# Kernel optimization log

Hardware: AMD Instinct MI355X
Metric: run time of the kernel (lower is better)

## Reference

```python
import jax, jax.numpy as jnp
import numpy as np

D_MODEL = 512
NUM_HEADS = 8
HEAD_DIM = D_MODEL // NUM_HEADS
BATCH = 4
SEQ = 2048
ROPE_BASE = 10000.0


def rope_cos_sin(seq_len, head_dim):
    inv_freq = 1.0 / (ROPE_BASE ** (jnp.arange(0, head_dim, 2, dtype=jnp.float32) / head_dim))
    t = jnp.arange(seq_len, dtype=jnp.float32)
    freqs = jnp.outer(t, inv_freq)              # (S, head_dim/2)
    emb = jnp.concatenate([freqs, freqs], axis=-1)  # (S, head_dim)
    return jnp.cos(emb), jnp.sin(emb)


def apply_rope(x, cos, sin):
    # x: (..., S, head_dim); cos/sin: (S, head_dim)
    x1 = x[..., ::2]
    x2 = x[..., 1::2]
    ch = cos[..., ::2]
    sh = sin[..., ::2]
    r1 = x1 * ch - x2 * sh
    r2 = x1 * sh + x2 * ch
    return jnp.stack([r1, r2], axis=-1).reshape(x.shape)


def setup_inputs() -> dict:
    key = jax.random.key(0)
    ks = jax.random.split(key, 12)
    x = jax.random.normal(ks[0], (BATCH, SEQ, D_MODEL), dtype=jnp.float32)
    variate_ids = jnp.sort(jax.random.randint(ks[1], (BATCH, SEQ), 0, 8), axis=-1).astype(jnp.int64)
    mask = jnp.ones((BATCH, SEQ), dtype=jnp.float32)
    s = 1.0 / np.sqrt(D_MODEL)
    Wq = jax.random.normal(ks[2], (D_MODEL, D_MODEL), dtype=jnp.float32) * s
    bq = jnp.zeros((D_MODEL,), dtype=jnp.float32)
    Wk = jax.random.normal(ks[3], (D_MODEL, D_MODEL), dtype=jnp.float32) * s
    bk = jnp.zeros((D_MODEL,), dtype=jnp.float32)
    Wv = jax.random.normal(ks[4], (D_MODEL, D_MODEL), dtype=jnp.float32) * s
    bv = jnp.zeros((D_MODEL,), dtype=jnp.float32)
    Wo = jax.random.normal(ks[5], (D_MODEL, D_MODEL), dtype=jnp.float32) * s
    bo = jnp.zeros((D_MODEL,), dtype=jnp.float32)
    u_same = jax.random.normal(ks[6], (NUM_HEADS,), dtype=jnp.float32) * 0.1
    u_cross = jax.random.normal(ks[7], (NUM_HEADS,), dtype=jnp.float32) * 0.1
    return dict(x=x, variate_ids=variate_ids, mask=mask, Wq=Wq, bq=bq, Wk=Wk, bk=bk,
                Wv=Wv, bv=bv, Wo=Wo, bo=bo, u_same=u_same, u_cross=u_cross)


def reference(x, variate_ids, mask, Wq, bq, Wk, bk, Wv, bv, Wo, bo, u_same, u_cross):
    B, S, D = x.shape
    H, Hd = NUM_HEADS, HEAD_DIM
    scale = 1.0 / np.sqrt(Hd)

    def proj(W, b):
        return (x @ W.T + b).reshape(B, S, H, Hd).transpose(0, 2, 1, 3)  # (B,H,S,Hd)

    q = proj(Wq, bq)
    k = proj(Wk, bk)
    v = proj(Wv, bv)

    cos, sin = rope_cos_sin(S, Hd)
    q = apply_rope(q, cos, sin)
    k = apply_rope(k, cos, sin)

    scores = jnp.einsum('bhid,bhjd->bhij', q, k) * scale  # (B,H,S,S)
    same = (variate_ids[:, :, None] == variate_ids[:, None, :]).astype(jnp.float32)  # (B,S,S)
    bias = same[:, None] * u_same[None, :, None, None] + (1.0 - same)[:, None] * u_cross[None, :, None, None]
    scores = scores + bias
    scores = scores + (1.0 - mask[:, None, None, :]) * -1e9
    probs = jax.nn.softmax(scores, axis=-1)
    out = jnp.einsum('bhij,bhjd->bhid', probs, v)  # (B,H,S,Hd)
    out = out.transpose(0, 2, 1, 3).reshape(B, S, D)
    return out @ Wo.T + bo
```

## Files before the change

### kernel.cpp

```cpp
#include <hip/hip_runtime.h>
#include <hip/hip_bf16.h>

#define BATCH   4
#define SEQ     2048
#define DMODEL  512
#define NHEADS  8
#define HEADDIM 64
#define MTOT    (BATCH*SEQ)
#define NX      (MTOT*DMODEL)
#define NW      (DMODEL*DMODEL)
#define QTILE   64
#define KTILE   32
#define NKT_G   32

#define LOG2E   1.4426950408889634f
#define SCL2    0.18033688011112042f
#define SHIFT   14.426950408889634f

typedef unsigned short u16;
typedef __bf16 bf16x8 __attribute__((ext_vector_type(8)));
typedef float  f32x4  __attribute__((ext_vector_type(4)));
typedef unsigned short u16x4 __attribute__((ext_vector_type(4)));
typedef unsigned u32x2 __attribute__((ext_vector_type(2)));

#define MFMA(a,b,c) __builtin_amdgcn_mfma_f32_16x16x32_bf16(a,b,c,0,0,0)

__device__ __forceinline__ u16 f2bf(float f) {
    unsigned u = __float_as_uint(f);
    u += 0x7FFFu + ((u >> 16) & 1u);
    return (u16)(u >> 16);
}
__device__ __forceinline__ unsigned pk_bf16(float a, float b) {
    union { __hip_bfloat162 h; unsigned u; } cv;
    cv.h = __float22bfloat162_rn(make_float2(a, b));
    return cv.u;
}
__device__ __forceinline__ float qsum16(float v) {
    v += __shfl_xor(v, 1);
    v += __shfl_xor(v, 2);
    v += __shfl_xor(v, 4);
    v += __shfl_xor(v, 8);
    return v;
}
__device__ __forceinline__ void gll16(const void* g, void* l) {
    __builtin_amdgcn_global_load_lds((const __attribute__((address_space(1))) void*)g,
                                     (__attribute__((address_space(3))) void*)l, 16, 0, 0);
}
__device__ __forceinline__ void gll4(const void* g, void* l) {
    __builtin_amdgcn_global_load_lds((const __attribute__((address_space(1))) void*)g,
                                     (__attribute__((address_space(3))) void*)l, 4, 0, 0);
}

#define NCVT4 ((NX + 4*NW)/4)
__global__ __launch_bounds__(256) void cvt_rope_kernel(
    const float* __restrict__ x,
    const float* __restrict__ wq, const float* __restrict__ wk,
    const float* __restrict__ wv, const float* __restrict__ wo,
    u16* __restrict__ xbf,
    u16* __restrict__ wqbf, u16* __restrict__ wkbf,
    u16* __restrict__ wvbf, u16* __restrict__ wobf,
    float2* __restrict__ cst)
{
    int i4 = blockIdx.x * 256 + threadIdx.x;
    if (i4 < NCVT4) {
        int i = i4 * 4;
        const float* s; u16* d; int o;
        if (i < NX) { s = x; d = xbf; o = i; }
        else {
            int j = i - NX;
            int r = j >> 18;
            o = j & (NW - 1);
            s = (r == 0) ? wq : (r == 1) ? wk : (r == 2) ? wv : wo;
            d = (r == 0) ? wqbf : (r == 1) ? wkbf : (r == 2) ? wvbf : wobf;
        }
        float4 v = *(const float4*)(s + o);
        u16x4 u = { f2bf(v.x), f2bf(v.y), f2bf(v.z), f2bf(v.w) };
        *(u16x4*)(d + o) = u;
    } else {
        int r = i4 - NCVT4;
        if (r < SEQ * 32 / 4) {
            int idx = r * 4;
            int s  = idx >> 5;
            int p0 = idx & 31;
#pragma unroll
            for (int t = 0; t < 4; ++t) {
                int p = p0 + t;
                float inv = __expf(-0.5756462732485115f * (float)(p & 15));
                float ang = (float)s * inv;
                cst[idx + t] = make_float2(cosf(ang), sinf(ang));
            }
        }
    }
}

#define TP 136
__global__ __launch_bounds__(256) void qkv_kernel(
    const u16* __restrict__ x,
    const u16* __restrict__ Wq, const float* __restrict__ bq,
    const u16* __restrict__ Wk, const float* __restrict__ bk,
    const u16* __restrict__ Wv, const float* __restrict__ bv,
    const float* __restrict__ cstf,
    u16* __restrict__ qws, u16* __restrict__ kws, u16* __restrict__ vtws)
{
    __shared__ alignas(16) u16 smem[128 * TP];
    u16* As = smem;
    u16* Bs = smem + 8192;

    const int m0 = blockIdx.x * 128;
    const int n0 = blockIdx.y * 128;
    const int tid  = threadIdx.x;
    const int w    = tid >> 6;
    const int lane = tid & 63;
    const int quad = lane >> 4;
    const int l16  = lane & 15;
    const int wm = w & 1, wn = w >> 1;

    const int sec = n0 >> 9;
    const int oc0 = n0 & 511;
    const u16*   Wm = (sec == 0) ? Wq : (sec == 1 ? Wk : Wv);
    const float* bb = (sec == 0) ? bq : (sec == 1 ? bk : bv);

    const int xb = (sec < 2) ? wn : wm;
    const int wb = (sec < 2) ? wm : wn;

    f32x4 acc[4][4] = {};

    for (int kb = 0; kb < 8; ++kb) {
#pragma unroll
        for (int it = 0; it < 4; ++it) {
            const int s   = it * 256 + tid;
            const int row = s >> 3;
            const int cb  = s & 7;
            const int gcol = kb * 64 + (((cb ^ (row & 7))) << 3);
            gll16(x  + (m0  + row) * 512 + gcol, &As[s * 8]);
            gll16(Wm + (oc0 + row) * 512 + gcol, &Bs[s * 8]);
        }
        __syncthreads();

#pragma unroll
        for (int ks = 0; ks < 2; ++ks) {
            bf16x8 xf[4], wf[4];
#pragma unroll
            for (int t = 0; t < 4; ++t) {
                const int xrow = xb * 64 + t * 16 + l16;
                const int wrow = wb * 64 + t * 16 + l16;
                xf[t] = *(const bf16x8*)&As[xrow * 64 + (((ks * 4 + quad) ^ (xrow & 7)) << 3)];
                wf[t] = *(const bf16x8*)&Bs[wrow * 64 + (((ks * 4 + quad) ^ (wrow & 7)) << 3)];
            }
            if (sec < 2) {
#pragma unroll
                for (int tm = 0; tm < 4; ++tm)
#pragma unroll
                    for (int tn = 0; tn < 4; ++tn)
                        acc[tm][tn] = MFMA(wf[tm], xf[tn], acc[tm][tn]);
            } else {
#pragma unroll
                for (int tm = 0; tm < 4; ++tm)
#pragma unroll
                    for (int tn = 0; tn < 4; ++tn)
                        acc[tm][tn] = MFMA(xf[tm], wf[tn], acc[tm][tn]);
            }
        }
        __syncthreads();
    }

    if (sec < 2) {
#pragma unroll
        for (int tm = 0; tm < 4; ++tm) {
            const int dls = wm * 64 + tm * 16 + quad * 4;
            const float4 bv4 = *(const float4*)&bb[oc0 + dls];
            const int pbase = ((oc0 + dls) & 63) >> 1;
#pragma unroll
            for (int tn = 0; tn < 4; ++tn) {
                const int sl = wn * 64 + tn * 16 + l16;
                const int sg = (m0 + sl) & 2047;
                const float4 cs = *(const float4*)&cstf[sg * 64 + pbase * 2];
                const float v0 = acc[tm][tn][0] + bv4.x;
                const float v1 = acc[tm][tn][1] + bv4.y;
                const float v2 = acc[tm][tn][2] + bv4.z;
                const float v3 = acc[tm][tn][3] + bv4.w;
                const float r0 = v0 * cs.x - v1 * cs.y;
                const float r1 = v1 * cs.x + v0 * cs.y;
                const float r2 = v2 * cs.z - v3 * cs.w;
                const float r3 = v3 * cs.z + v2 * cs.w;
                u32x2 pv = { pk_bf16(r0, r1), pk_bf16(r2, r3) };
                *(u32x2*)&smem[sl * TP + dls] = pv;
            }
        }
        __syncthreads();
        u16* dst0 = (sec == 0) ? qws : kws;
#pragma unroll
        for (int i = 0; i < 8; ++i) {
            const int c   = i * 256 + tid;
            const int sl  = c >> 4;
            const int d8  = (c & 15) * 8;
            const int gcol = oc0 + d8;
            const int hh  = gcol >> 6;
            const int dh  = gcol & 63;
            const int sgl = m0 + sl;
            const int bi  = sgl >> 11;
            const int s   = sgl & 2047;
            u16* dst = dst0 + (size_t)(bi * NHEADS + hh) * (SEQ * HEADDIM)
                            + (size_t)s * HEADDIM + dh;
            *(bf16x8*)dst = *(const bf16x8*)&smem[sl * TP + d8];
        }
    } else {
#pragma unroll
        for (int tm = 0; tm < 4; ++tm) {
            const int row_l = wm * 64 + tm * 16 + quad * 4;
#pragma unroll
            for (int tn = 0; tn < 4; ++tn) {
                const int col_l = wn * 64 + tn * 16 + l16;
                const float bval = bb[oc0 + col_l];
                u32x2 pv = { pk_bf16(acc[tm][tn][0] + bval, acc[tm][tn][1] + bval),
                             pk_bf16(acc[tm][tn][2] + bval, acc[tm][tn][3] + bval) };
                *(u32x2*)&smem[col_l * TP + row_l] = pv;
            }
        }
        __syncthreads();
        const int bi  = m0 >> 11;
        const int sgb = m0 & 2047;
#pragma unroll
        for (int i = 0; i < 8; ++i) {
            const int c    = i * 256 + tid;
            const int col  = c >> 4;
            const int sc8  = (c & 15) * 8;
            const int gcol = oc0 + col;
            const int hh   = gcol >> 6;
            const int d    = gcol & 63;
            u16* dst = vtws + (size_t)(bi * NHEADS + hh) * (SEQ * HEADDIM)
                            + (size_t)d * SEQ + sgb + sc8;
            *(bf16x8*)dst = *(const bf16x8*)&smem[col * TP + sc8];
        }
    }
}

__global__ __launch_bounds__(512, 6) void attn_kernel(
    const u16* __restrict__ qws, const u16* __restrict__ kws,
    const u16* __restrict__ vtl,
    const int* __restrict__ vids, const float* __restrict__ mask,
    const float* __restrict__ u_same, const float* __restrict__ u_cross,
    u16* __restrict__ attn)
{
    __shared__ alignas(16) u16 smem[21504];
    __shared__ int   bidm[2][2][KTILE];
    __shared__ float bmkm[2][2][KTILE];
    __shared__ float comb_li[QTILE];

    const int bh = blockIdx.y;
    const int b  = bh >> 3;
    const int h  = bh & 7;
    const int q0 = blockIdx.x * QTILE;

    const int tid  = threadIdx.x;
    const int w    = tid >> 6;
    const int lane = tid & 63;
    const int quad = lane >> 4;
    const int l16  = lane & 15;
    const int qw   = w & 3;
    const int kg   = w >> 2;
    const int tl   = tid & 255;

    const float us2 = u_same[h]  * LOG2E;
    const float uc2 = u_cross[h] * LOG2E;
    const size_t tb = (size_t)bh * (SEQ * HEADDIM);

    const int qr = q0 + qw * 16 + l16;
    const bf16x8 aq0 = *(const bf16x8*)(qws + tb + qr * HEADDIM + quad * 8);
    const bf16x8 aq1 = *(const bf16x8*)(qws + tb + qr * HEADDIM + 32 + quad * 8);

    int vq[4];
#pragma unroll
    for (int r = 0; r < 4; ++r)
        vq[r] = vids[b * SEQ + q0 + qw * 16 + quad * 4 + r];

    float li[4] = {0.f, 0.f, 0.f, 0.f};
    f32x4 o[4] = {};

    const int srow  = tl >> 3;
    const int scb   = tl & 7;
    const int soff  = ((scb ^ (srow & 7)) << 3);
    const int vrow  = tl >> 2;
    const int vcb   = tl & 3;
    const int soffv = ((vcb ^ (vrow & 3)) << 3);
    const int kbase = kg * 2 * 2048;

    auto stage = [&](int t, int nb) {
        const int k0 = (kg * NKT_G + t) * KTILE;
        gll16(kws + tb + (size_t)(k0 + srow) * HEADDIM + soff,
              &smem[kbase + nb * 2048 + tl * 8]);
        gll16(vtl + tb + (size_t)vrow * SEQ + k0 + soffv,
              &smem[8192 + kbase + nb * 2048 + tl * 8]);
        if (tl < KTILE) {
            gll4(vids + b * SEQ + k0 + tl, &bidm[kg][nb][0]);
            gll4(mask + b * SEQ + k0 + tl, &bmkm[kg][nb][0]);
        }
    };

    u16* const pls = &smem[16384 + w * 640];

    auto body = [&](const int cur) {
        const u16* kb_b = &smem[kbase + cur * 2048];
        const u16* vb_b = &smem[8192 + kbase + cur * 2048];
#pragma unroll
        for (int nt = 0; nt < 2; ++nt) {
            const int krow = nt * 16 + l16;
            const int r7   = krow & 7;
            const bf16x8 kb0 = *(const bf16x8*)&kb_b[krow * 64 + ((quad ^ r7) << 3)];
            const bf16x8 kb1 = *(const bf16x8*)&kb_b[krow * 64 + ((quad ^ r7 ^ 4) << 3)];
            f32x4 sc = {};
            sc = MFMA(aq0, kb0, sc);
            sc = MFMA(aq1, kb1, sc);
            const int   kv  = bidm[kg][cur][krow];
            const float mdl = fmaf(bmkm[kg][cur][krow], 1.4426950408889634e9f,
                                   -1.4426950408889634e9f - SHIFT);
            const float as_ = us2 + mdl;
            const float ac_ = uc2 + mdl;
            float p[4];
#pragma unroll
            for (int r = 0; r < 4; ++r) {
                const float sel = (kv == vq[r]) ? as_ : ac_;
                p[r] = __builtin_amdgcn_exp2f(fmaf(sc[r], SCL2, sel));
                li[r] += p[r];
            }
            const unsigned p01 = pk_bf16(p[0], p[1]);
            const unsigned p23 = pk_bf16(p[2], p[3]);
            u16* pb = &pls[(quad * 4) * 40 + nt * 16 + l16];
            pb[0]   = (u16)p01;  pb[40]  = (u16)(p01 >> 16);
            pb[80]  = (u16)p23;  pb[120] = (u16)(p23 >> 16);
        }

        const bf16x8 ap0 = *(const bf16x8*)&pls[l16 * 40 + quad * 8];

#pragma unroll
        for (int nt = 0; nt < 4; ++nt) {
            const int vr = nt * 16 + l16;
            const bf16x8 vb0 = *(const bf16x8*)&vb_b[vr * 32 + ((quad ^ (vr & 3)) << 3)];
            o[nt] = MFMA(ap0, vb0, o[nt]);
        }
    };

    stage(0, 0);
    for (int t = 0; t < NKT_G; t += 2) {
        __syncthreads();
        stage(t + 1, 1);
        body(0);
        __syncthreads();
        if (t + 2 < NKT_G) stage(t + 2, 0);
        body(1);
    }

    __syncthreads();
    float* co = (float*)smem;
    if (kg == 1) {
#pragma unroll
        for (int r = 0; r < 4; ++r) {
            const float liq = qsum16(li[r]);
            if (l16 == 0) comb_li[qw * 16 + quad * 4 + r] = liq;
        }
#pragma unroll
        for (int nt = 0; nt < 4; ++nt)
#pragma unroll
            for (int r = 0; r < 4; ++r)
                co[(qw * 16 + quad * 4 + r) * 65 + nt * 16 + l16] = o[nt][r];
    }
    __syncthreads();
    if (kg == 0) {
#pragma unroll
        for (int r = 0; r < 4; ++r) {
            const int qloc = qw * 16 + quad * 4 + r;
            const float lt = qsum16(li[r]) + comb_li[qloc];
            const float inv = 1.0f / lt;
            const int R  = q0 + qloc;
            const int rb = (b * SEQ + R) * DMODEL + h * HEADDIM;
#pragma unroll
            for (int nt = 0; nt < 4; ++nt)
                attn[rb + nt * 16 + l16] =
                    f2bf((o[nt][r] + co[qloc * 65 + nt * 16 + l16]) * inv);
        }
    }
}

__global__ __launch_bounds__(256) void proj_kernel(
    const u16* __restrict__ a, const u16* __restrict__ Wo,
    const float* __restrict__ bo, float* __restrict__ out)
{
    __shared__ alignas(16) u16 psm[132 * 64 * 2];
    u16* As = psm;
    u16* Bs = psm + 8192;
    float* Lp = (float*)psm;

    const int m0 = blockIdx.x * 128;
    const int n0 = blockIdx.y * 128;
    const int tid  = threadIdx.x;
    const int w    = tid >> 6;
    const int lane = tid & 63;
    const int quad = lane >> 4;
    const int l16  = lane & 15;
    const int wm = w & 1, wn = w >> 1;

    f32x4 acc[4][4] = {};

    for (int kb = 0; kb < 8; ++kb) {
#pragma unroll
        for (int it = 0; it < 4; ++it) {
            const int s   = it * 256 + tid;
            const int row = s >> 3;
            const int cb  = s & 7;
            const int gcol = kb * 64 + (((cb ^ (row & 7))) << 3);
            gll16(a  + (m0 + row) * 512 + gcol, &As[s * 8]);
            gll16(Wo + (n0 + row) * 512 + gcol, &Bs[s * 8]);
        }
        __syncthreads();

#pragma unroll
        for (int ks = 0; ks < 2; ++ks) {
            bf16x8 af[4], wf[4];
#pragma unroll
            for (int t = 0; t < 4; ++t) {
                const int arow = wn * 64 + t * 16 + l16;
                const int wrow = wm * 64 + t * 16 + l16;
                af[t] = *(const bf16x8*)&As[arow * 64 + (((ks * 4 + quad) ^ (arow & 7)) << 3)];
                wf[t] = *(const bf16x8*)&Bs[wrow * 64 + (((ks * 4 + quad) ^ (wrow & 7)) << 3)];
            }
#pragma unroll
            for (int tm = 0; tm < 4; ++tm)
#pragma unroll
                for (int tn = 0; tn < 4; ++tn)
                    acc[tm][tn] = MFMA(wf[tm], af[tn], acc[tm][tn]);
        }
        __syncthreads();
    }

#pragma unroll
    for (int hph = 0; hph < 2; ++hph) {
        if (wn == hph) {
#pragma unroll
            for (int tm = 0; tm < 4; ++tm) {
                const int dls = wm * 64 + tm * 16 + quad * 4;
                const float4 bv4 = *(const float4*)&bo[n0 + dls];
#pragma unroll
                for (int tn = 0; tn < 4; ++tn) {
                    const int s2 = tn * 16 + l16;
                    float4 v = { acc[tm][tn][0] + bv4.x, acc[tm][tn][1] + bv4.y,
                                 acc[tm][tn][2] + bv4.z, acc[tm][tn][3] + bv4.w };
                    *(float4*)&Lp[s2 * 132 + dls] = v;
                }
            }
        }
        __syncthreads();
#pragma unroll
        for (int i = 0; i < 8; ++i) {
            const int c  = i * 256 + tid;
            const int s2 = c >> 5;
            const int dq = (c & 31) * 4;
            float4 v = *(const float4*)&Lp[s2 * 132 + dq];
            *(float4*)&out[(size_t)(m0 + hph * 64 + s2) * 512 + n0 + dq] = v;
        }
        __syncthreads();
    }
}

extern "C" void kernel_launch(void* const* d_in, const int* in_sizes, int n_in,
                              void* d_out, int out_size, void* d_ws, size_t ws_size,
                              hipStream_t stream) {
    const float* x    = (const float*)d_in[0];
    const int*   vids = (const int*)d_in[1];
    const float* mask = (const float*)d_in[2];
    const float* Wq = (const float*)d_in[3];
    const float* bq = (const float*)d_in[4];
    const float* Wk = (const float*)d_in[5];
    const float* bk = (const float*)d_in[6];
    const float* Wv = (const float*)d_in[7];
    const float* bv = (const float*)d_in[8];
    const float* Wo = (const float*)d_in[9];
    const float* bo = (const float*)d_in[10];
    const float* usame  = (const float*)d_in[11];
    const float* ucross = (const float*)d_in[12];
    float* out = (float*)d_out;

    u16* xbf  = (u16*)d_ws;
    u16* wqbf = xbf + NX;
    u16* wkbf = wqbf + NW;
    u16* wvbf = wkbf + NW;
    u16* wobf = wvbf + NW;
    float2* cst = (float2*)(wobf + NW);
    u16* qws  = (u16*)(cst + SEQ * 32);
    u16* kws  = qws + (size_t)BATCH * NHEADS * SEQ * HEADDIM;
    u16* vtws = kws + (size_t)BATCH * NHEADS * SEQ * HEADDIM;
    u16* attn = xbf;

    cvt_rope_kernel<<<(NCVT4 + SEQ * 32 / 4 + 255) / 256, 256, 0, stream>>>(
        x, Wq, Wk, Wv, Wo, xbf, wqbf, wkbf, wvbf, wobf, cst);

    dim3 g1(MTOT / 128, 3 * DMODEL / 128);
    qkv_kernel<<<g1, 256, 0, stream>>>(xbf, wqbf, bq, wkbf, bk, wvbf, bv,
                                       (const float*)cst, qws, kws, vtws);

    dim3 g2(SEQ / QTILE, BATCH * NHEADS);
    attn_kernel<<<g2, 512, 0, stream>>>(qws, kws, vtws, vids, mask,
                                        usame, ucross, attn);

    dim3 g3(MTOT / 128, DMODEL / 128);
    proj_kernel<<<g3, 256, 0, stream>>>(attn, wobf, bo, out);
}
```

Baseline: 203.9 us.

## Compute transposed scores and build P operand via lane shuffles instead of LDS

The QK^T MFMA operands are swapped so each lane holds scores for one query row across four keys. The bf16 probability A-operand for the PV MFMA is then assembled with cross-lane shuffles rather than a round trip through a per-wave LDS scratch buffer. This removes the P staging LDS, shrinking shared memory and allowing launch bounds to request 8 waves per SIMD instead of 6. The V LDS swizzle is also changed. Row sums reduce over fewer shuffles. The cost is extra shuffle and select instructions plus possible register pressure at the higher occupancy target.

Result: slower. 336.8 us (+65.1%).

```diff
diff --git a/kernel.cpp b/kernel.cpp
--- a/kernel.cpp
+++ b/kernel.cpp
@@ -34,13 +34,6 @@
     union { __hip_bfloat162 h; unsigned u; } cv;
     cv.h = __float22bfloat162_rn(make_float2(a, b));
     return cv.u;
-}
-__device__ __forceinline__ float qsum16(float v) {
-    v += __shfl_xor(v, 1);
-    v += __shfl_xor(v, 2);
-    v += __shfl_xor(v, 4);
-    v += __shfl_xor(v, 8);
-    return v;
 }
 __device__ __forceinline__ void gll16(const void* g, void* l) {
     __builtin_amdgcn_global_load_lds((const __attribute__((address_space(1))) void*)g,
@@ -235,17 +228,17 @@
     }
 }
 
-__global__ __launch_bounds__(512, 6) void attn_kernel(
+__global__ __launch_bounds__(512, 8) void attn_kernel(
     const u16* __restrict__ qws, const u16* __restrict__ kws,
     const u16* __restrict__ vtl,
     const int* __restrict__ vids, const float* __restrict__ mask,
     const float* __restrict__ u_same, const float* __restrict__ u_cross,
     u16* __restrict__ attn)
 {
-    __shared__ alignas(16) u16 smem[21504];
+    __shared__ alignas(16) u16 smem[16384];
     __shared__ int   bidm[2][2][KTILE];
     __shared__ float bmkm[2][2][KTILE];
-    __shared__ float comb_li[QTILE];
+    __shared__ float comb_li2[2][QTILE];
 
     const int bh = blockIdx.y;
     const int b  = bh >> 3;
@@ -269,20 +262,17 @@
     const bf16x8 aq0 = *(const bf16x8*)(qws + tb + qr * HEADDIM + quad * 8);
     const bf16x8 aq1 = *(const bf16x8*)(qws + tb + qr * HEADDIM + 32 + quad * 8);
 
-    int vq[4];
-#pragma unroll
-    for (int r = 0; r < 4; ++r)
-        vq[r] = vids[b * SEQ + q0 + qw * 16 + quad * 4 + r];
-
-    float li[4] = {0.f, 0.f, 0.f, 0.f};
+    const int vq = vids[b * SEQ + q0 + qw * 16 + l16];
+
+    float li = 0.f;
     f32x4 o[4] = {};
 
     const int srow  = tl >> 3;
     const int scb   = tl & 7;
     const int soff  = ((scb ^ (srow & 7)) << 3);
     const int vrow  = tl >> 2;
-    const int vcb   = tl & 3;
-    const int soffv = ((vcb ^ (vrow & 3)) << 3);
+    const int vcb   = (tl & 3) ^ ((vrow >> 1) & 3);
+    const int soffv = (vcb << 3);
     const int kbase = kg * 2 * 2048;
 
     auto stage = [&](int t, int nb) {
@@ -297,11 +287,10 @@
         }
     };
 
-    u16* const pls = &smem[16384 + w * 640];
-
     auto body = [&](const int cur) {
         const u16* kb_b = &smem[kbase + cur * 2048];
         const u16* vb_b = &smem[8192 + kbase + cur * 2048];
+        unsigned x0, x1, y0, y1;
 #pragma unroll
         for (int nt = 0; nt < 2; ++nt) {
             const int krow = nt * 16 + l16;
@@ -309,34 +298,45 @@
             const bf16x8 kb0 = *(const bf16x8*)&kb_b[krow * 64 + ((quad ^ r7) << 3)];
             const bf16x8 kb1 = *(const bf16x8*)&kb_b[krow * 64 + ((quad ^ r7 ^ 4) << 3)];
             f32x4 sc = {};
-            sc = MFMA(aq0, kb0, sc);
-            sc = MFMA(aq1, kb1, sc);
-            const int   kv  = bidm[kg][cur][krow];
-            const float mdl = fmaf(bmkm[kg][cur][krow], 1.4426950408889634e9f,
-                                   -1.4426950408889634e9f - SHIFT);
-            const float as_ = us2 + mdl;
-            const float ac_ = uc2 + mdl;
+            sc = MFMA(kb0, aq0, sc);
+            sc = MFMA(kb1, aq1, sc);
+            const int kk = nt * 16 + quad * 4;
+            const int4   kv4 = *(const int4*)&bidm[kg][cur][kk];
+            const float4 mk4 = *(const float4*)&bmkm[kg][cur][kk];
+            const int   kvr[4] = { kv4.x, kv4.y, kv4.z, kv4.w };
+            const float mkr[4] = { mk4.x, mk4.y, mk4.z, mk4.w };
             float p[4];
 #pragma unroll
             for (int r = 0; r < 4; ++r) {
-                const float sel = (kv == vq[r]) ? as_ : ac_;
+                const float mdl = fmaf(mkr[r], 1.4426950408889634e9f,
+                                       -1.4426950408889634e9f - SHIFT);
+                const float sel = (kvr[r] == vq) ? (us2 + mdl) : (uc2 + mdl);
                 p[r] = __builtin_amdgcn_exp2f(fmaf(sc[r], SCL2, sel));
-                li[r] += p[r];
-            }
-            const unsigned p01 = pk_bf16(p[0], p[1]);
-            const unsigned p23 = pk_bf16(p[2], p[3]);
-            u16* pb = &pls[(quad * 4) * 40 + nt * 16 + l16];
-            pb[0]   = (u16)p01;  pb[40]  = (u16)(p01 >> 16);
-            pb[80]  = (u16)p23;  pb[120] = (u16)(p23 >> 16);
-        }
-
-        const bf16x8 ap0 = *(const bf16x8*)&pls[l16 * 40 + quad * 8];
+                li += p[r];
+            }
+            if (nt == 0) { x0 = pk_bf16(p[0], p[1]); x1 = pk_bf16(p[2], p[3]); }
+            else         { y0 = pk_bf16(p[0], p[1]); y1 = pk_bf16(p[2], p[3]); }
+        }
+
+        const bool qlo = (quad < 2);
+        const bool qod = (quad & 1);
+        const unsigned a0 = qlo ? x0 : y0, a1 = qlo ? x1 : y1;
+        const unsigned r0 = __shfl_xor((int)a0, 16), r1 = __shfl_xor((int)a1, 16);
+        const unsigned b0 = qod ? x0 : y0, b1 = qod ? x1 : y1;
+        const unsigned s0 = __shfl_xor((int)b0, 32), s1 = __shfl_xor((int)b1, 32);
+        const unsigned c0 = qod ? y0 : x0, c1 = qod ? y1 : x1;
+        const unsigned t0 = __shfl_xor((int)c0, 48), t1 = __shfl_xor((int)c1, 48);
+        union { unsigned u[4]; bf16x8 v; } ap;
+        ap.u[0] = (quad == 0) ? x0 : (quad == 1) ? t0 : (quad == 2) ? s0 : r0;
+        ap.u[1] = (quad == 0) ? x1 : (quad == 1) ? t1 : (quad == 2) ? s1 : r1;
+        ap.u[2] = (quad == 0) ? r0 : (quad == 1) ? s0 : (quad == 2) ? t0 : y0;
+        ap.u[3] = (quad == 0) ? r1 : (quad == 1) ? s1 : (quad == 2) ? t1 : y1;
 
 #pragma unroll
         for (int nt = 0; nt < 4; ++nt) {
             const int vr = nt * 16 + l16;
-            const bf16x8 vb0 = *(const bf16x8*)&vb_b[vr * 32 + ((quad ^ (vr & 3)) << 3)];
-            o[nt] = MFMA(ap0, vb0, o[nt]);
+            const bf16x8 vb0 = *(const bf16x8*)&vb_b[vr * 32 + (((quad ^ ((vr >> 1) & 3))) << 3)];
+            o[nt] = MFMA(ap.v, vb0, o[nt]);
         }
     };
 
@@ -350,14 +350,12 @@
         body(1);
     }
 
+    float liq = li + __shfl_xor(li, 16);
+    liq += __shfl_xor(liq, 32);
     __syncthreads();
     float* co = (float*)smem;
+    if (quad == 0) comb_li2[kg][qw * 16 + l16] = liq;
     if (kg == 1) {
-#pragma unroll
-        for (int r = 0; r < 4; ++r) {
-            const float liq = qsum16(li[r]);
-            if (l16 == 0) comb_li[qw * 16 + quad * 4 + r] = liq;
-        }
 #pragma unroll
         for (int nt = 0; nt < 4; ++nt)
 #pragma unroll
@@ -369,7 +367,7 @@
 #pragma unroll
         for (int r = 0; r < 4; ++r) {
             const int qloc = qw * 16 + quad * 4 + r;
-            const float lt = qsum16(li[r]) + comb_li[qloc];
+            const float lt = comb_li2[0][qloc] + comb_li2[1][qloc];
             const float inv = 1.0f / lt;
             const int R  = q0 + qloc;
             const int rb = (b * SEQ + R) * DMODEL + h * HEADDIM;
```
